# Performance work log

Measured on AMD Instinct MI355X. Metric: run time of the kernel, lower is better.

## Reference

```python
import jax, jax.numpy as jnp
import numpy as np
import math

INPUT_SIZE = 512
DK = 64
B, N = 8, 2048

def setup_inputs() -> dict:
    key = jax.random.key(0)
    k1, k2, k3, k4, k5, k6 = jax.random.split(key, 6)
    X = jax.random.normal(k1, (B, N, INPUT_SIZE), dtype=jnp.float32)
    h = jax.random.normal(k2, (B, N, INPUT_SIZE), dtype=jnp.float32)
    s = 1.0 / math.sqrt(INPUT_SIZE)
    WQ = jax.random.uniform(k3, (INPUT_SIZE, DK), dtype=jnp.float32, minval=-s, maxval=s)
    bQ = jax.random.uniform(k4, (DK,), dtype=jnp.float32, minval=-s, maxval=s)
    WK = jax.random.uniform(k5, (INPUT_SIZE, DK), dtype=jnp.float32, minval=-s, maxval=s)
    bK = jax.random.uniform(k6, (DK,), dtype=jnp.float32, minval=-s, maxval=s)
    return {"X": X, "h": h, "WQ": WQ, "bQ": bQ, "WK": WK, "bK": bK}

def reference(X, h, WQ, bQ, WK, bK):
    # Q = linearQ(h), K = linearK(X); dropout is eval-mode identity
    Q = jnp.einsum('bnd,dk->bnk', h, WQ) + bQ   # [B, N, dk]
    K = jnp.einsum('bnd,dk->bnk', X, WK) + bK   # [B, N, dk]
    scores = jnp.einsum('bqk,bnk->bqn', Q, K) / jnp.sqrt(jnp.asarray(DK, X.dtype))
    A = jax.nn.softmax(scores, axis=-1)          # [B, N, N]
    out = jnp.einsum('bqn,bnd->bqd', A, X)       # V = X
    return out
```

## Files before the change

kernel.cpp:

```cpp
#include <hip/hip_runtime.h>
#include <hip/hip_bf16.h>

#define B_ 8
#define N_ 2048
#define D_ 512
#define DK_ 64

typedef float f32x4 __attribute__((ext_vector_type(4)));
typedef short bf16x8 __attribute__((ext_vector_type(8)));
typedef unsigned short u16;

__device__ __forceinline__ u16 f2bf(float f) {
  union { float f; unsigned u; } v; v.f = f;
  unsigned r = v.u + 0x7FFFu + ((v.u >> 16) & 1u);
  return (u16)(r >> 16);
}

#define MFMA16(a, b, cacc) __builtin_amdgcn_mfma_f32_16x16x32_bf16((a), (b), (cacc), 0, 0, 0)


__global__ __launch_bounds__(256) void vt_kernel(const float* __restrict__ X,
                                                 u16* __restrict__ Vf) {
  int bid = blockIdx.x;
  int dt = bid & 7, nt = (bid >> 3) & 31, b = bid >> 8;
  int n0 = nt * 64, d0 = dt * 64;
  __shared__ u16 T[64 * 72];
  int t = threadIdx.x;
  const float* Xb = X + ((size_t)b * N_ + n0) * D_ + d0;
#pragma unroll
  for (int p = 0; p < 4; ++p) {
    int r = p * 16 + (t >> 4);
    int c4 = (t & 15) * 4;
    f32x4 v = *reinterpret_cast<const f32x4*>(Xb + (size_t)r * D_ + c4);
#pragma unroll
    for (int j = 0; j < 4; ++j) T[(c4 + j) * 72 + r] = f2bf(v[j]);
  }
  __syncthreads();
  int w = t >> 6, l = t & 63, g = l >> 4, c = l & 15;
#pragma unroll
  for (int ks = 0; ks < 2; ++ks) {
    bf16x8 v = *reinterpret_cast<const bf16x8*>(&T[(w * 16 + c) * 72 + ks * 32 + 8 * g]);
    *reinterpret_cast<bf16x8*>(
        Vf + (((size_t)(b * 32 + dt * 4 + w) * 32 + nt) * 2 + ks) * 512 + l * 8) = v;
  }
}

__global__ __launch_bounds__(256) void proj_kernel(
    const float* __restrict__ h, const float* __restrict__ X,
    const float* __restrict__ WQ, const float* __restrict__ bQ,
    const float* __restrict__ WK, const float* __restrict__ bK,
    u16* __restrict__ Qf, u16* __restrict__ Kf) {
  int bid = blockIdx.x;
  int b = bid & 7, nt = bid >> 3;
  int n0 = nt * 64;
  int t = threadIdx.x, w = t >> 6, l = t & 63, g = l >> 4, c = l & 15;
  int arow = n0 + w * 16 + c;
  const float* hrow = h + ((size_t)b * N_ + arow) * D_;
  const float* Xrow = X + ((size_t)b * N_ + arow) * D_;
  f32x4 accq[4], acck[4];
#pragma unroll
  for (int cf = 0; cf < 4; ++cf) {
    accq[cf] = (f32x4){0.f, 0.f, 0.f, 0.f};
    acck[cf] = (f32x4){0.f, 0.f, 0.f, 0.f};
  }
  for (int k0 = 0; k0 < D_; k0 += 32) {
    bf16x8 ah, ax;
    {
      f32x4 h0 = *reinterpret_cast<const f32x4*>(hrow + k0 + 8 * g);
      f32x4 h1 = *reinterpret_cast<const f32x4*>(hrow + k0 + 8 * g + 4);
      f32x4 x0 = *reinterpret_cast<const f32x4*>(Xrow + k0 + 8 * g);
      f32x4 x1 = *reinterpret_cast<const f32x4*>(Xrow + k0 + 8 * g + 4);
#pragma unroll
      for (int i = 0; i < 4; ++i) {
        ah[i] = (short)f2bf(h0[i]); ah[i + 4] = (short)f2bf(h1[i]);
        ax[i] = (short)f2bf(x0[i]); ax[i + 4] = (short)f2bf(x1[i]);
      }
    }
#pragma unroll
    for (int cf = 0; cf < 4; ++cf) {
      bf16x8 bq, bk;
#pragma unroll
      for (int i = 0; i < 8; ++i) {
        int kk = k0 + 8 * g + i;
        bq[i] = (short)f2bf(WQ[(size_t)kk * DK_ + cf * 16 + c]);
        bk[i] = (short)f2bf(WK[(size_t)kk * DK_ + cf * 16 + c]);
      }
      accq[cf] = MFMA16(ah, bq, accq[cf]);
      acck[cf] = MFMA16(ax, bk, acck[cf]);
    }
  }
#pragma unroll
  for (int cf = 0; cf < 4; ++cf) {
    float vq = bQ[cf * 16 + c], vk = bK[cf * 16 + c];
    int ks = cf >> 1;
    int g2 = ((cf & 1) * 16 + c) >> 3;
    int i2 = c & 7;
#pragma unroll
    for (int r = 0; r < 4; ++r) {
      size_t e = ((size_t)(b * 128 + nt * 4 + w) * 2 + ks) * 512 +
                 (g2 * 16 + 4 * g + r) * 8 + i2;
      Qf[e] = f2bf((accq[cf][r] + vq) * 0.125f);
      Kf[e] = f2bf(acck[cf][r] + vk);
    }
  }
}

__global__ __launch_bounds__(512, 1) void attn_kernel(
    const u16* __restrict__ Qf, const u16* __restrict__ Kf,
    const u16* __restrict__ Vf, float* __restrict__ out) {
  int bid = blockIdx.x;
  int b = bid & 7, qt = bid >> 3;
  int q0 = qt * 64;
  int t = threadIdx.x, w = t >> 6, l = t & 63, g = l >> 4, c = l & 15;
  int qh = w >> 2, kq = w & 3;

  __shared__ u16 Plds[2][64][72];
  __shared__ float Lp[4][64];

  bf16x8 aq[2][2];
#pragma unroll
  for (int qf = 0; qf < 2; ++qf)
#pragma unroll
    for (int ks = 0; ks < 2; ++ks)
      aq[qf][ks] = *reinterpret_cast<const bf16x8*>(
          Qf + ((size_t)(b * 128 + qt * 4 + qh * 2 + qf) * 2 + ks) * 512 + l * 8);

  f32x4 o[4][4];
#pragma unroll
  for (int a = 0; a < 4; ++a)
#pragma unroll
    for (int d = 0; d < 4; ++d) o[a][d] = (f32x4){0.f, 0.f, 0.f, 0.f};
  float lp[2][4];
#pragma unroll
  for (int a = 0; a < 2; ++a)
#pragma unroll
    for (int r = 0; r < 4; ++r) lp[a][r] = 0.f;

  const u16* Kbase = Kf + (size_t)(b * 128 + kq) * 2 * 512 + l * 8;
  const u16* Vbase = Vf + ((size_t)(b * 32 + w * 4) * 32) * 2 * 512 + l * 8;

  bf16x8 vA[8], vB[8], kA[2], kB[2];
#pragma unroll
  for (int ks = 0; ks < 2; ++ks) {
    kA[ks] = *reinterpret_cast<const bf16x8*>(Kbase + (size_t)ks * 512);
#pragma unroll
    for (int df = 0; df < 4; ++df)
      vA[ks * 4 + df] = *reinterpret_cast<const bf16x8*>(
          Vbase + ((size_t)df * 32 * 2 + ks) * 512);
  }

  auto body = [&](bf16x8 (&vC)[8], bf16x8 (&kC)[2],
                  bf16x8 (&vN)[8], bf16x8 (&kN)[2], int i) {
    const int pb = i & 1;
    const int kvn = (i + 1) & 31;

    f32x4 s0 = (f32x4){0.f, 0.f, 0.f, 0.f};
    f32x4 s1 = (f32x4){0.f, 0.f, 0.f, 0.f};
    s0 = MFMA16(aq[0][0], kC[0], s0); s0 = MFMA16(aq[0][1], kC[1], s0);
    s1 = MFMA16(aq[1][0], kC[0], s1); s1 = MFMA16(aq[1][1], kC[1], s1);

#pragma unroll
    for (int r = 0; r < 4; ++r) {
      float p0 = __expf(s0[r]); lp[0][r] += p0;
      Plds[pb][qh * 32 + 4 * g + r][kq * 16 + c] = f2bf(p0);
      float p1 = __expf(s1[r]); lp[1][r] += p1;
      Plds[pb][qh * 32 + 16 + 4 * g + r][kq * 16 + c] = f2bf(p1);
    }

    __syncthreads();

#pragma unroll
    for (int ks = 0; ks < 2; ++ks)
      kN[ks] = *reinterpret_cast<const bf16x8*>(
          Kbase + ((size_t)kvn * 4 * 2 + ks) * 512);
#pragma unroll
    for (int ks = 0; ks < 2; ++ks)
#pragma unroll
      for (int df = 0; df < 4; ++df)
        vN[ks * 4 + df] = *reinterpret_cast<const bf16x8*>(
            Vbase + (((size_t)df * 32 + kvn) * 2 + ks) * 512);

    bf16x8 pa0, pa1, pa2, pa3;
    __builtin_amdgcn_s_setprio(1);
#pragma unroll
    for (int ks = 0; ks < 2; ++ks) {
      pa0 = *reinterpret_cast<const bf16x8*>(&Plds[pb][c][ks * 32 + 8 * g]);
      pa1 = *reinterpret_cast<const bf16x8*>(&Plds[pb][16 + c][ks * 32 + 8 * g]);
      pa2 = *reinterpret_cast<const bf16x8*>(&Plds[pb][32 + c][ks * 32 + 8 * g]);
      pa3 = *reinterpret_cast<const bf16x8*>(&Plds[pb][48 + c][ks * 32 + 8 * g]);
#pragma unroll
      for (int df = 0; df < 4; ++df) {
        o[0][df] = MFMA16(pa0, vC[ks * 4 + df], o[0][df]);
        o[1][df] = MFMA16(pa1, vC[ks * 4 + df], o[1][df]);
        o[2][df] = MFMA16(pa2, vC[ks * 4 + df], o[2][df]);
        o[3][df] = MFMA16(pa3, vC[ks * 4 + df], o[3][df]);
      }
    }
    __builtin_amdgcn_s_setprio(0);
  };

#pragma unroll 1
  for (int i = 0; i < 32; i += 2) {
    body(vA, kA, vB, kB, i);
    body(vB, kB, vA, kA, i + 1);
  }

#pragma unroll
  for (int qf = 0; qf < 2; ++qf)
#pragma unroll
    for (int r = 0; r < 4; ++r) {
      float v = lp[qf][r];
      v += __shfl_xor(v, 1); v += __shfl_xor(v, 2);
      v += __shfl_xor(v, 4); v += __shfl_xor(v, 8);
      lp[qf][r] = v;
    }
  if (c == 0) {
#pragma unroll
    for (int qf = 0; qf < 2; ++qf)
#pragma unroll
      for (int r = 0; r < 4; ++r)
        Lp[kq][qh * 32 + qf * 16 + 4 * g + r] = lp[qf][r];
  }
  __syncthreads();

  float* outb = out + ((size_t)b * N_ + q0) * D_;
#pragma unroll
  for (int qf2 = 0; qf2 < 4; ++qf2)
#pragma unroll
    for (int r = 0; r < 4; ++r) {
      int ql = qf2 * 16 + 4 * g + r;
      float L = Lp[0][ql] + Lp[1][ql] + Lp[2][ql] + Lp[3][ql];
      float inv = 1.0f / L;
#pragma unroll
      for (int df = 0; df < 4; ++df)
        outb[(size_t)ql * D_ + w * 64 + df * 16 + c] = o[qf2][df][r] * inv;
    }
}

extern "C" void kernel_launch(void* const* d_in, const int* in_sizes, int n_in,
                              void* d_out, int out_size, void* d_ws, size_t ws_size,
                              hipStream_t stream) {
  const float* X  = (const float*)d_in[0];
  const float* h  = (const float*)d_in[1];
  const float* WQ = (const float*)d_in[2];
  const float* bQ = (const float*)d_in[3];
  const float* WK = (const float*)d_in[4];
  const float* bK = (const float*)d_in[5];
  float* out = (float*)d_out;

  u16* Vf = (u16*)d_ws;
  u16* Qf = Vf + (size_t)B_ * D_ * N_;
  u16* Kf = Qf + (size_t)B_ * N_ * DK_;

  vt_kernel<<<dim3(2048), dim3(256), 0, stream>>>(X, Vf);
  proj_kernel<<<dim3(256), dim3(256), 0, stream>>>(h, X, WQ, bQ, WK, bK, Qf, Kf);
  attn_kernel<<<dim3(256), dim3(512), 0, stream>>>(Qf, Kf, Vf, out);
}
```

Before: 81.23 us.

## Split attention output dimension across two blocks of four waves each

The attention kernel now launches 512 blocks of 256 threads instead of 256 blocks of 512, with each block covering half of the 512-wide value/output dimension. Each wave computes a 32x32 score tile instead of 32x16. The P tile row stride is padded to 76 to reduce LDS bank conflicts. This raises block count to fill more CUs and allows two blocks per CU, at the cost of each block recomputing the full QK^T scores and exponentials for its half, doubling that work overall.

```diff
diff --git a/kernel.cpp b/kernel.cpp
--- a/kernel.cpp
+++ b/kernel.cpp
@@ -105,17 +105,17 @@
   }
 }
 
-__global__ __launch_bounds__(512, 1) void attn_kernel(
+__global__ __launch_bounds__(256, 2) void attn_kernel(
     const u16* __restrict__ Qf, const u16* __restrict__ Kf,
     const u16* __restrict__ Vf, float* __restrict__ out) {
   int bid = blockIdx.x;
-  int b = bid & 7, qt = bid >> 3;
+  int b = bid & 7, dh = (bid >> 3) & 1, qt = bid >> 4;
   int q0 = qt * 64;
   int t = threadIdx.x, w = t >> 6, l = t & 63, g = l >> 4, c = l & 15;
-  int qh = w >> 2, kq = w & 3;
-
-  __shared__ u16 Plds[2][64][72];
-  __shared__ float Lp[4][64];
+  int qh = w >> 1, kq = w & 1;
+
+  __shared__ u16 Plds[2][64][76];
+  __shared__ float Lp[2][64];
 
   bf16x8 aq[2][2];
 #pragma unroll
@@ -136,43 +136,57 @@
 #pragma unroll
     for (int r = 0; r < 4; ++r) lp[a][r] = 0.f;
 
-  const u16* Kbase = Kf + (size_t)(b * 128 + kq) * 2 * 512 + l * 8;
-  const u16* Vbase = Vf + ((size_t)(b * 32 + w * 4) * 32) * 2 * 512 + l * 8;
-
-  bf16x8 vA[8], vB[8], kA[2], kB[2];
-#pragma unroll
-  for (int ks = 0; ks < 2; ++ks) {
-    kA[ks] = *reinterpret_cast<const bf16x8*>(Kbase + (size_t)ks * 512);
+  const u16* Kbase = Kf + (size_t)(b * 128 + kq * 2) * 2 * 512 + l * 8;
+  const u16* Vbase = Vf + ((size_t)(b * 32 + dh * 16 + w * 4) * 32) * 2 * 512 + l * 8;
+
+  bf16x8 vA[8], vB[8], kA[4], kB[4];
+#pragma unroll
+  for (int kf = 0; kf < 2; ++kf)
+#pragma unroll
+    for (int ks = 0; ks < 2; ++ks)
+      kA[kf * 2 + ks] = *reinterpret_cast<const bf16x8*>(
+          Kbase + ((size_t)kf * 2 + ks) * 512);
+#pragma unroll
+  for (int ks = 0; ks < 2; ++ks)
 #pragma unroll
     for (int df = 0; df < 4; ++df)
       vA[ks * 4 + df] = *reinterpret_cast<const bf16x8*>(
           Vbase + ((size_t)df * 32 * 2 + ks) * 512);
-  }
-
-  auto body = [&](bf16x8 (&vC)[8], bf16x8 (&kC)[2],
-                  bf16x8 (&vN)[8], bf16x8 (&kN)[2], int i) {
+
+  auto body = [&](bf16x8 (&vC)[8], bf16x8 (&kC)[4],
+                  bf16x8 (&vN)[8], bf16x8 (&kN)[4], int i) {
     const int pb = i & 1;
     const int kvn = (i + 1) & 31;
 
-    f32x4 s0 = (f32x4){0.f, 0.f, 0.f, 0.f};
-    f32x4 s1 = (f32x4){0.f, 0.f, 0.f, 0.f};
-    s0 = MFMA16(aq[0][0], kC[0], s0); s0 = MFMA16(aq[0][1], kC[1], s0);
-    s1 = MFMA16(aq[1][0], kC[0], s1); s1 = MFMA16(aq[1][1], kC[1], s1);
-
-#pragma unroll
-    for (int r = 0; r < 4; ++r) {
-      float p0 = __expf(s0[r]); lp[0][r] += p0;
-      Plds[pb][qh * 32 + 4 * g + r][kq * 16 + c] = f2bf(p0);
-      float p1 = __expf(s1[r]); lp[1][r] += p1;
-      Plds[pb][qh * 32 + 16 + 4 * g + r][kq * 16 + c] = f2bf(p1);
-    }
+    f32x4 s[2][2];
+#pragma unroll
+    for (int qf = 0; qf < 2; ++qf)
+#pragma unroll
+      for (int kf = 0; kf < 2; ++kf) {
+        s[qf][kf] = (f32x4){0.f, 0.f, 0.f, 0.f};
+        s[qf][kf] = MFMA16(aq[qf][0], kC[kf * 2 + 0], s[qf][kf]);
+        s[qf][kf] = MFMA16(aq[qf][1], kC[kf * 2 + 1], s[qf][kf]);
+      }
+
+#pragma unroll
+    for (int qf = 0; qf < 2; ++qf)
+#pragma unroll
+      for (int kf = 0; kf < 2; ++kf)
+#pragma unroll
+        for (int r = 0; r < 4; ++r) {
+          float p = __expf(s[qf][kf][r]);
+          lp[qf][r] += p;
+          Plds[pb][qh * 32 + qf * 16 + 4 * g + r][kq * 32 + kf * 16 + c] = f2bf(p);
+        }
 
     __syncthreads();
 
 #pragma unroll
-    for (int ks = 0; ks < 2; ++ks)
-      kN[ks] = *reinterpret_cast<const bf16x8*>(
-          Kbase + ((size_t)kvn * 4 * 2 + ks) * 512);
+    for (int kf = 0; kf < 2; ++kf)
+#pragma unroll
+      for (int ks = 0; ks < 2; ++ks)
+        kN[kf * 2 + ks] = *reinterpret_cast<const bf16x8*>(
+            Kbase + ((size_t)(kvn * 4 + kf) * 2 + ks) * 512);
 #pragma unroll
     for (int ks = 0; ks < 2; ++ks)
 #pragma unroll
@@ -223,13 +237,13 @@
   }
   __syncthreads();
 
-  float* outb = out + ((size_t)b * N_ + q0) * D_;
+  float* outb = out + ((size_t)b * N_ + q0) * D_ + dh * 256;
 #pragma unroll
   for (int qf2 = 0; qf2 < 4; ++qf2)
 #pragma unroll
     for (int r = 0; r < 4; ++r) {
       int ql = qf2 * 16 + 4 * g + r;
-      float L = Lp[0][ql] + Lp[1][ql] + Lp[2][ql] + Lp[3][ql];
+      float L = Lp[0][ql] + Lp[1][ql];
       float inv = 1.0f / L;
 #pragma unroll
       for (int df = 0; df < 4; ++df)
@@ -254,5 +268,5 @@
 
   vt_kernel<<<dim3(2048), dim3(256), 0, stream>>>(X, Vf);
   proj_kernel<<<dim3(256), dim3(256), 0, stream>>>(h, X, WQ, bQ, WK, bK, Qf, Kf);
-  attn_kernel<<<dim3(256), dim3(512), 0, stream>>>(Qf, Kf, Vf, out);
-}
+  attn_kernel<<<dim3(512), dim3(256), 0, stream>>>(Qf, Kf, Vf, out);
+}
```

New measurement: 84.67 us. 4.2% more time.

## Software-pipeline QK^T of next tile with PV of current tile in attention

Applied to the files above, without the earlier changes.

Restructures the attention loop so that each iteration computes the scores and exp for tile i+1 into one P buffer while doing the PV MFMAs for tile i from the other buffer, with a prologue and epilogue peeling. K is prefetched two tiles ahead and V one tile ahead. The LDS row pitch changes from 72 to 76 to alter bank mapping. This is meant to overlap the exp/VALU work with the matrix work and hide the barrier, at the cost of more live registers and an extra sync.

```diff
diff --git a/kernel.cpp b/kernel.cpp
--- a/kernel.cpp
+++ b/kernel.cpp
@@ -114,7 +114,7 @@
   int t = threadIdx.x, w = t >> 6, l = t & 63, g = l >> 4, c = l & 15;
   int qh = w >> 2, kq = w & 3;
 
-  __shared__ u16 Plds[2][64][72];
+  __shared__ u16 Plds[2][64][76];
   __shared__ float Lp[4][64];
 
   bf16x8 aq[2][2];
@@ -140,69 +140,108 @@
   const u16* Vbase = Vf + ((size_t)(b * 32 + w * 4) * 32) * 2 * 512 + l * 8;
 
   bf16x8 vA[8], vB[8], kA[2], kB[2];
-#pragma unroll
-  for (int ks = 0; ks < 2; ++ks) {
+
+#pragma unroll
+  for (int ks = 0; ks < 2; ++ks)
     kA[ks] = *reinterpret_cast<const bf16x8*>(Kbase + (size_t)ks * 512);
+#pragma unroll
+  for (int ks = 0; ks < 2; ++ks)
 #pragma unroll
     for (int df = 0; df < 4; ++df)
       vA[ks * 4 + df] = *reinterpret_cast<const bf16x8*>(
           Vbase + ((size_t)df * 32 * 2 + ks) * 512);
-  }
-
-  auto body = [&](bf16x8 (&vC)[8], bf16x8 (&kC)[2],
-                  bf16x8 (&vN)[8], bf16x8 (&kN)[2], int i) {
-    const int pb = i & 1;
-    const int kvn = (i + 1) & 31;
-
+#pragma unroll
+  for (int ks = 0; ks < 2; ++ks)
+    kB[ks] = *reinterpret_cast<const bf16x8*>(Kbase + ((size_t)4 * 2 + ks) * 512);
+  {
     f32x4 s0 = (f32x4){0.f, 0.f, 0.f, 0.f};
     f32x4 s1 = (f32x4){0.f, 0.f, 0.f, 0.f};
-    s0 = MFMA16(aq[0][0], kC[0], s0); s0 = MFMA16(aq[0][1], kC[1], s0);
-    s1 = MFMA16(aq[1][0], kC[0], s1); s1 = MFMA16(aq[1][1], kC[1], s1);
-
+    s0 = MFMA16(aq[0][0], kA[0], s0); s0 = MFMA16(aq[0][1], kA[1], s0);
+    s1 = MFMA16(aq[1][0], kA[0], s1); s1 = MFMA16(aq[1][1], kA[1], s1);
 #pragma unroll
     for (int r = 0; r < 4; ++r) {
       float p0 = __expf(s0[r]); lp[0][r] += p0;
-      Plds[pb][qh * 32 + 4 * g + r][kq * 16 + c] = f2bf(p0);
+      Plds[0][qh * 32 + 4 * g + r][kq * 16 + c] = f2bf(p0);
       float p1 = __expf(s1[r]); lp[1][r] += p1;
-      Plds[pb][qh * 32 + 16 + 4 * g + r][kq * 16 + c] = f2bf(p1);
-    }
-
-    __syncthreads();
+      Plds[0][qh * 32 + 16 + 4 * g + r][kq * 16 + c] = f2bf(p1);
+    }
+  }
+  __syncthreads();
+
+  auto body = [&](bf16x8 (&vCur)[8], bf16x8 (&vNxt)[8],
+                  bf16x8 (&kS)[2], bf16x8 (&kL)[2], int i) {
+    const int pbW = (i + 1) & 1, pbR = i & 1;
+    const int kv1 = (i + 1) & 31;
+    const int kv2 = (i + 2) & 31;
 
 #pragma unroll
     for (int ks = 0; ks < 2; ++ks)
-      kN[ks] = *reinterpret_cast<const bf16x8*>(
-          Kbase + ((size_t)kvn * 4 * 2 + ks) * 512);
+      kL[ks] = *reinterpret_cast<const bf16x8*>(
+          Kbase + ((size_t)kv2 * 4 * 2 + ks) * 512);
 #pragma unroll
     for (int ks = 0; ks < 2; ++ks)
 #pragma unroll
       for (int df = 0; df < 4; ++df)
-        vN[ks * 4 + df] = *reinterpret_cast<const bf16x8*>(
-            Vbase + (((size_t)df * 32 + kvn) * 2 + ks) * 512);
+        vNxt[ks * 4 + df] = *reinterpret_cast<const bf16x8*>(
+            Vbase + (((size_t)df * 32 + kv1) * 2 + ks) * 512);
+
+    f32x4 s0 = (f32x4){0.f, 0.f, 0.f, 0.f};
+    f32x4 s1 = (f32x4){0.f, 0.f, 0.f, 0.f};
+    s0 = MFMA16(aq[0][0], kS[0], s0); s0 = MFMA16(aq[0][1], kS[1], s0);
+    s1 = MFMA16(aq[1][0], kS[0], s1); s1 = MFMA16(aq[1][1], kS[1], s1);
+
+#pragma unroll
+    for (int r = 0; r < 4; ++r) {
+      float p0 = __expf(s0[r]); lp[0][r] += p0;
+      Plds[pbW][qh * 32 + 4 * g + r][kq * 16 + c] = f2bf(p0);
+      float p1 = __expf(s1[r]); lp[1][r] += p1;
+      Plds[pbW][qh * 32 + 16 + 4 * g + r][kq * 16 + c] = f2bf(p1);
+    }
 
     bf16x8 pa0, pa1, pa2, pa3;
     __builtin_amdgcn_s_setprio(1);
 #pragma unroll
     for (int ks = 0; ks < 2; ++ks) {
-      pa0 = *reinterpret_cast<const bf16x8*>(&Plds[pb][c][ks * 32 + 8 * g]);
-      pa1 = *reinterpret_cast<const bf16x8*>(&Plds[pb][16 + c][ks * 32 + 8 * g]);
-      pa2 = *reinterpret_cast<const bf16x8*>(&Plds[pb][32 + c][ks * 32 + 8 * g]);
-      pa3 = *reinterpret_cast<const bf16x8*>(&Plds[pb][48 + c][ks * 32 + 8 * g]);
+      pa0 = *reinterpret_cast<const bf16x8*>(&Plds[pbR][c][ks * 32 + 8 * g]);
+      pa1 = *reinterpret_cast<const bf16x8*>(&Plds[pbR][16 + c][ks * 32 + 8 * g]);
+      pa2 = *reinterpret_cast<const bf16x8*>(&Plds[pbR][32 + c][ks * 32 + 8 * g]);
+      pa3 = *reinterpret_cast<const bf16x8*>(&Plds[pbR][48 + c][ks * 32 + 8 * g]);
 #pragma unroll
       for (int df = 0; df < 4; ++df) {
-        o[0][df] = MFMA16(pa0, vC[ks * 4 + df], o[0][df]);
-        o[1][df] = MFMA16(pa1, vC[ks * 4 + df], o[1][df]);
-        o[2][df] = MFMA16(pa2, vC[ks * 4 + df], o[2][df]);
-        o[3][df] = MFMA16(pa3, vC[ks * 4 + df], o[3][df]);
+        o[0][df] = MFMA16(pa0, vCur[ks * 4 + df], o[0][df]);
+        o[1][df] = MFMA16(pa1, vCur[ks * 4 + df], o[1][df]);
+        o[2][df] = MFMA16(pa2, vCur[ks * 4 + df], o[2][df]);
+        o[3][df] = MFMA16(pa3, vCur[ks * 4 + df], o[3][df]);
       }
     }
     __builtin_amdgcn_s_setprio(0);
+
+    __syncthreads();
   };
 
 #pragma unroll 1
-  for (int i = 0; i < 32; i += 2) {
-    body(vA, kA, vB, kB, i);
-    body(vB, kB, vA, kA, i + 1);
+  for (int i = 0; i < 30; i += 2) {
+    body(vA, vB, kB, kA, i);
+    body(vB, vA, kA, kB, i + 1);
+  }
+  body(vA, vB, kB, kA, 30);
+
+  {
+    bf16x8 pa0, pa1, pa2, pa3;
+#pragma unroll
+    for (int ks = 0; ks < 2; ++ks) {
+      pa0 = *reinterpret_cast<const bf16x8*>(&Plds[1][c][ks * 32 + 8 * g]);
+      pa1 = *reinterpret_cast<const bf16x8*>(&Plds[1][16 + c][ks * 32 + 8 * g]);
+      pa2 = *reinterpret_cast<const bf16x8*>(&Plds[1][32 + c][ks * 32 + 8 * g]);
+      pa3 = *reinterpret_cast<const bf16x8*>(&Plds[1][48 + c][ks * 32 + 8 * g]);
+#pragma unroll
+      for (int df = 0; df < 4; ++df) {
+        o[0][df] = MFMA16(pa0, vB[ks * 4 + df], o[0][df]);
+        o[1][df] = MFMA16(pa1, vB[ks * 4 + df], o[1][df]);
+        o[2][df] = MFMA16(pa2, vB[ks * 4 + df], o[2][df]);
+        o[3][df] = MFMA16(pa3, vB[ks * 4 + df], o[3][df]);
+      }
+    }
   }
 
 #pragma unroll
@@ -214,6 +253,7 @@
       v += __shfl_xor(v, 4); v += __shfl_xor(v, 8);
       lp[qf][r] = v;
     }
+  __syncthreads();
   if (c == 0) {
 #pragma unroll
     for (int qf = 0; qf < 2; ++qf)
```

New measurement: 82.01 us. No clear change (+1.0%).

## Software-pipeline attention with 32-wide KV steps and one barrier per step

Applied to the files above, without the earlier changes.

The attention kernel now walks KV in 32-key tiles (64 steps) instead of 64-key tiles. Each step computes the scores and exp for the next tile while running the P·V MFMAs on the previous tile from a double-buffered LDS slot. K and V registers are rotated across four buffers, so global loads are issued three tiles ahead. The aim is to overlap softmax, LDS traffic and global loads with the P·V matrix work and to halve the barrier span, at the cost of more loop iterations, more barriers in total and higher register pressure.

```diff
diff --git a/kernel.cpp b/kernel.cpp
--- a/kernel.cpp
+++ b/kernel.cpp
@@ -17,6 +17,12 @@
 }
 
 #define MFMA16(a, b, cacc) __builtin_amdgcn_mfma_f32_16x16x32_bf16((a), (b), (cacc), 0, 0, 0)
+
+#define BARRIER_LGKM() do {                                   \
+    asm volatile("s_waitcnt lgkmcnt(0)" ::: "memory");        \
+    __builtin_amdgcn_s_barrier();                             \
+    asm volatile("" ::: "memory");                            \
+  } while (0)
 
 
 __global__ __launch_bounds__(256) void vt_kernel(const float* __restrict__ X,
@@ -112,114 +118,128 @@
   int b = bid & 7, qt = bid >> 3;
   int q0 = qt * 64;
   int t = threadIdx.x, w = t >> 6, l = t & 63, g = l >> 4, c = l & 15;
-  int qh = w >> 2, kq = w & 3;
-
-  __shared__ u16 Plds[2][64][72];
-  __shared__ float Lp[4][64];
-
-  bf16x8 aq[2][2];
-#pragma unroll
-  for (int qf = 0; qf < 2; ++qf)
+  int qh = w >> 1, kq = w & 1;
+
+  __shared__ u16 Plds[2][64][40];
+  __shared__ float Lp[2][64];
+
+  bf16x8 aq[2];
+#pragma unroll
+  for (int ks = 0; ks < 2; ++ks)
+    aq[ks] = *reinterpret_cast<const bf16x8*>(
+        Qf + ((size_t)(b * 128 + qt * 4 + qh) * 2 + ks) * 512 + l * 8);
+
+  f32x4 o[4][4];
+#pragma unroll
+  for (int a = 0; a < 4; ++a)
+#pragma unroll
+    for (int d = 0; d < 4; ++d) o[a][d] = (f32x4){0.f, 0.f, 0.f, 0.f};
+  float lp[4] = {0.f, 0.f, 0.f, 0.f};
+
+  const u16* Kbase = Kf + ((size_t)(b * 256 + 2 * kq)) * 512 + l * 8;
+  const u16* Vbase = Vf + ((size_t)(b * 32 + w * 4) * 64) * 512 + l * 8;
+
+  bf16x8 kbuf[4][2], vbuf[4][4];
+
+#pragma unroll
+  for (int j = 0; j < 3; ++j) {
 #pragma unroll
     for (int ks = 0; ks < 2; ++ks)
-      aq[qf][ks] = *reinterpret_cast<const bf16x8*>(
-          Qf + ((size_t)(b * 128 + qt * 4 + qh * 2 + qf) * 2 + ks) * 512 + l * 8);
-
-  f32x4 o[4][4];
-#pragma unroll
-  for (int a = 0; a < 4; ++a)
-#pragma unroll
-    for (int d = 0; d < 4; ++d) o[a][d] = (f32x4){0.f, 0.f, 0.f, 0.f};
-  float lp[2][4];
-#pragma unroll
-  for (int a = 0; a < 2; ++a)
-#pragma unroll
-    for (int r = 0; r < 4; ++r) lp[a][r] = 0.f;
-
-  const u16* Kbase = Kf + (size_t)(b * 128 + kq) * 2 * 512 + l * 8;
-  const u16* Vbase = Vf + ((size_t)(b * 32 + w * 4) * 32) * 2 * 512 + l * 8;
-
-  bf16x8 vA[8], vB[8], kA[2], kB[2];
-#pragma unroll
-  for (int ks = 0; ks < 2; ++ks) {
-    kA[ks] = *reinterpret_cast<const bf16x8*>(Kbase + (size_t)ks * 512);
-#pragma unroll
-    for (int df = 0; df < 4; ++df)
-      vA[ks * 4 + df] = *reinterpret_cast<const bf16x8*>(
-          Vbase + ((size_t)df * 32 * 2 + ks) * 512);
-  }
-
-  auto body = [&](bf16x8 (&vC)[8], bf16x8 (&kC)[2],
-                  bf16x8 (&vN)[8], bf16x8 (&kN)[2], int i) {
-    const int pb = i & 1;
-    const int kvn = (i + 1) & 31;
-
-    f32x4 s0 = (f32x4){0.f, 0.f, 0.f, 0.f};
-    f32x4 s1 = (f32x4){0.f, 0.f, 0.f, 0.f};
-    s0 = MFMA16(aq[0][0], kC[0], s0); s0 = MFMA16(aq[0][1], kC[1], s0);
-    s1 = MFMA16(aq[1][0], kC[0], s1); s1 = MFMA16(aq[1][1], kC[1], s1);
-
-#pragma unroll
-    for (int r = 0; r < 4; ++r) {
-      float p0 = __expf(s0[r]); lp[0][r] += p0;
-      Plds[pb][qh * 32 + 4 * g + r][kq * 16 + c] = f2bf(p0);
-      float p1 = __expf(s1[r]); lp[1][r] += p1;
-      Plds[pb][qh * 32 + 16 + 4 * g + r][kq * 16 + c] = f2bf(p1);
-    }
-
-    __syncthreads();
+      kbuf[j][ks] = *reinterpret_cast<const bf16x8*>(
+          Kbase + (size_t)(4 * j + ks) * 512);
+#pragma unroll
+    for (int f = 0; f < 4; ++f)
+      vbuf[j][f] = *reinterpret_cast<const bf16x8*>(
+          Vbase + (size_t)(f * 64 + j) * 512);
+  }
+  {
+    f32x4 s = (f32x4){0.f, 0.f, 0.f, 0.f};
+    s = MFMA16(aq[0], kbuf[0][0], s);
+    s = MFMA16(aq[1], kbuf[0][1], s);
+#pragma unroll
+    for (int r = 0; r < 4; ++r) {
+      float p = __expf(s[r]); lp[r] += p;
+      Plds[0][qh * 16 + 4 * g + r][kq * 16 + c] = f2bf(p);
+    }
+  }
+  BARRIER_LGKM();
+
+  auto body = [&](bf16x8 (&kS)[2], bf16x8 (&kL)[2],
+                  bf16x8 (&vR)[4], bf16x8 (&vL)[4], int i) {
+    const int kvL = (i + 3) & 63;
+    const int pbW = (i + 1) & 1, pbR = i & 1;
 
 #pragma unroll
     for (int ks = 0; ks < 2; ++ks)
-      kN[ks] = *reinterpret_cast<const bf16x8*>(
-          Kbase + ((size_t)kvn * 4 * 2 + ks) * 512);
-#pragma unroll
-    for (int ks = 0; ks < 2; ++ks)
-#pragma unroll
-      for (int df = 0; df < 4; ++df)
-        vN[ks * 4 + df] = *reinterpret_cast<const bf16x8*>(
-            Vbase + (((size_t)df * 32 + kvn) * 2 + ks) * 512);
-
-    bf16x8 pa0, pa1, pa2, pa3;
+      kL[ks] = *reinterpret_cast<const bf16x8*>(
+          Kbase + (size_t)(4 * kvL + ks) * 512);
+#pragma unroll
+    for (int f = 0; f < 4; ++f)
+      vL[f] = *reinterpret_cast<const bf16x8*>(
+          Vbase + (size_t)(f * 64 + kvL) * 512);
+
+    f32x4 s = (f32x4){0.f, 0.f, 0.f, 0.f};
+    s = MFMA16(aq[0], kS[0], s);
+    s = MFMA16(aq[1], kS[1], s);
+
+#pragma unroll
+    for (int r = 0; r < 4; ++r) {
+      float p = __expf(s[r]); lp[r] += p;
+      Plds[pbW][qh * 16 + 4 * g + r][kq * 16 + c] = f2bf(p);
+    }
+
+    bf16x8 pa0 = *reinterpret_cast<const bf16x8*>(&Plds[pbR][c][8 * g]);
+    bf16x8 pa1 = *reinterpret_cast<const bf16x8*>(&Plds[pbR][16 + c][8 * g]);
+    bf16x8 pa2 = *reinterpret_cast<const bf16x8*>(&Plds[pbR][32 + c][8 * g]);
+    bf16x8 pa3 = *reinterpret_cast<const bf16x8*>(&Plds[pbR][48 + c][8 * g]);
     __builtin_amdgcn_s_setprio(1);
 #pragma unroll
-    for (int ks = 0; ks < 2; ++ks) {
-      pa0 = *reinterpret_cast<const bf16x8*>(&Plds[pb][c][ks * 32 + 8 * g]);
-      pa1 = *reinterpret_cast<const bf16x8*>(&Plds[pb][16 + c][ks * 32 + 8 * g]);
-      pa2 = *reinterpret_cast<const bf16x8*>(&Plds[pb][32 + c][ks * 32 + 8 * g]);
-      pa3 = *reinterpret_cast<const bf16x8*>(&Plds[pb][48 + c][ks * 32 + 8 * g]);
-#pragma unroll
-      for (int df = 0; df < 4; ++df) {
-        o[0][df] = MFMA16(pa0, vC[ks * 4 + df], o[0][df]);
-        o[1][df] = MFMA16(pa1, vC[ks * 4 + df], o[1][df]);
-        o[2][df] = MFMA16(pa2, vC[ks * 4 + df], o[2][df]);
-        o[3][df] = MFMA16(pa3, vC[ks * 4 + df], o[3][df]);
-      }
+    for (int dt = 0; dt < 4; ++dt) {
+      o[0][dt] = MFMA16(pa0, vR[dt], o[0][dt]);
+      o[1][dt] = MFMA16(pa1, vR[dt], o[1][dt]);
+      o[2][dt] = MFMA16(pa2, vR[dt], o[2][dt]);
+      o[3][dt] = MFMA16(pa3, vR[dt], o[3][dt]);
     }
     __builtin_amdgcn_s_setprio(0);
+
+    BARRIER_LGKM();
   };
 
 #pragma unroll 1
-  for (int i = 0; i < 32; i += 2) {
-    body(vA, kA, vB, kB, i);
-    body(vB, kB, vA, kA, i + 1);
-  }
-
-#pragma unroll
-  for (int qf = 0; qf < 2; ++qf)
-#pragma unroll
-    for (int r = 0; r < 4; ++r) {
-      float v = lp[qf][r];
-      v += __shfl_xor(v, 1); v += __shfl_xor(v, 2);
-      v += __shfl_xor(v, 4); v += __shfl_xor(v, 8);
-      lp[qf][r] = v;
-    }
+  for (int i = 0; i < 60; i += 4) {
+    body(kbuf[1], kbuf[3], vbuf[0], vbuf[3], i);
+    body(kbuf[2], kbuf[0], vbuf[1], vbuf[0], i + 1);
+    body(kbuf[3], kbuf[1], vbuf[2], vbuf[1], i + 2);
+    body(kbuf[0], kbuf[2], vbuf[3], vbuf[2], i + 3);
+  }
+  body(kbuf[1], kbuf[3], vbuf[0], vbuf[3], 60);
+  body(kbuf[2], kbuf[0], vbuf[1], vbuf[0], 61);
+  body(kbuf[3], kbuf[1], vbuf[2], vbuf[1], 62);
+
+  {
+    bf16x8 pa0 = *reinterpret_cast<const bf16x8*>(&Plds[1][c][8 * g]);
+    bf16x8 pa1 = *reinterpret_cast<const bf16x8*>(&Plds[1][16 + c][8 * g]);
+    bf16x8 pa2 = *reinterpret_cast<const bf16x8*>(&Plds[1][32 + c][8 * g]);
+    bf16x8 pa3 = *reinterpret_cast<const bf16x8*>(&Plds[1][48 + c][8 * g]);
+#pragma unroll
+    for (int dt = 0; dt < 4; ++dt) {
+      o[0][dt] = MFMA16(pa0, vbuf[3][dt], o[0][dt]);
+      o[1][dt] = MFMA16(pa1, vbuf[3][dt], o[1][dt]);
+      o[2][dt] = MFMA16(pa2, vbuf[3][dt], o[2][dt]);
+      o[3][dt] = MFMA16(pa3, vbuf[3][dt], o[3][dt]);
+    }
+  }
+
+#pragma unroll
+  for (int r = 0; r < 4; ++r) {
+    float v = lp[r];
+    v += __shfl_xor(v, 1); v += __shfl_xor(v, 2);
+    v += __shfl_xor(v, 4); v += __shfl_xor(v, 8);
+    lp[r] = v;
+  }
   if (c == 0) {
 #pragma unroll
-    for (int qf = 0; qf < 2; ++qf)
-#pragma unroll
-      for (int r = 0; r < 4; ++r)
-        Lp[kq][qh * 32 + qf * 16 + 4 * g + r] = lp[qf][r];
+    for (int r = 0; r < 4; ++r) Lp[kq][qh * 16 + 4 * g + r] = lp[r];
   }
   __syncthreads();
 
@@ -229,7 +249,7 @@
 #pragma unroll
     for (int r = 0; r < 4; ++r) {
       int ql = qf2 * 16 + 4 * g + r;
-      float L = Lp[0][ql] + Lp[1][ql] + Lp[2][ql] + Lp[3][ql];
+      float L = Lp[0][ql] + Lp[1][ql];
       float inv = 1.0f / L;
 #pragma unroll
       for (int df = 0; df < 4; ++df)
```

Result: no change. 80.51 us (-0.9%).
